# Kernel tuning notes

Measured on AMD Instinct MI355X. Metric: run time of the kernel, lower is better.

## Reference

```python
import jax, jax.numpy as jnp
import numpy as np

N = 100000   # nodes
E = 1600000  # edges
D = 128      # in_dim
H = 128      # hidden


def setup_inputs() -> dict:
    key = jax.random.key(0)
    k = jax.random.split(key, 6)
    x = jax.random.normal(k[0], (N, D), dtype=jnp.float32)
    edge_index = jax.random.randint(k[1], (2, E), 0, N, dtype=jnp.int64)
    s1 = 1.0 / np.sqrt(D)
    s2 = 1.0 / np.sqrt(H)
    W1 = jax.random.uniform(k[2], (D, H), jnp.float32, -s1, s1)
    b1 = jax.random.uniform(k[3], (H,), jnp.float32, -s1, s1)
    W2 = jax.random.uniform(k[4], (H, H), jnp.float32, -s2, s2)
    b2 = jax.random.uniform(k[5], (H,), jnp.float32, -s2, s2)
    return {"x": x, "W1": W1, "b1": b1, "W2": W2, "b2": b2,
            "edge_index": edge_index}


def reference(x, W1, b1, W2, b2, edge_index):
    n = x.shape[0]
    loop = jnp.arange(n, dtype=edge_index.dtype)
    src = jnp.concatenate([edge_index[0], loop])  # sources incl. self-loops
    dst = jnp.concatenate([edge_index[1], loop])  # targets incl. self-loops
    # symmetric GCN normalization: D^-1/2 A_hat D^-1/2
    deg = jax.ops.segment_sum(jnp.ones_like(dst, jnp.float32), dst,
                              num_segments=n)
    dinv = jnp.where(deg > 0, deg ** -0.5, 0.0)
    norm = dinv[src] * dinv[dst]  # [E+N]

    def gcn_conv(h, W, b):
        m = h @ W                                   # [N, H] transform first
        agg = jax.ops.segment_sum(norm[:, None] * m[src], dst,
                                  num_segments=n)   # gather-scale-scatter
        return agg + b

    h = jax.nn.relu(gcn_conv(x, W1, b1))  # dropout is identity in eval mode
    return gcn_conv(h, W2, b2)
```

## Files before the change

kernel.cpp:

```cpp
#include <hip/hip_runtime.h>


#define RB    9
#define RANGE 512
#define CAPB  16384
#define CHUNK 8192

typedef __attribute__((ext_vector_type(8))) short bf16x8;
typedef __attribute__((ext_vector_type(4))) float f32x4;

__device__ inline float bf_lo(unsigned w) { return __uint_as_float(w << 16); }
__device__ inline float bf_hi(unsigned w) { return __uint_as_float(w & 0xffff0000u); }
__device__ inline unsigned bf16pair(float lo, float hi) {
    unsigned a = __float_as_uint(lo), b = __float_as_uint(hi);
    a += 0x7fffu + ((a >> 16) & 1u);
    b += 0x7fffu + ((b >> 16) & 1u);
    return (a >> 16) | (b & 0xffff0000u);
}
__device__ inline unsigned short bf16rne(float f) {
    unsigned u = __float_as_uint(f);
    u += 0x7fffu + ((u >> 16) & 1u);
    return (unsigned short)(u >> 16);
}
__device__ inline float bf2f(unsigned short h) { return __uint_as_float(((unsigned)h) << 16); }

__device__ inline void pack_one(int idx, const float* __restrict__ W,
                                uint4* __restrict__ Bhi, uint4* __restrict__ Blo) {
    int lane = idx & 63, ks = (idx >> 6) & 3, nt = idx >> 8;
    int j = nt * 16 + (lane & 15);
    int k0 = ks * 32 + ((lane >> 4) & 3) * 8;
    unsigned hi[4], lo[4];
#pragma unroll
    for (int p = 0; p < 4; p++) {
        float w0 = W[(size_t)(k0 + 2 * p) * 128 + j];
        float w1 = W[(size_t)(k0 + 2 * p + 1) * 128 + j];
        unsigned short h0 = bf16rne(w0), h1 = bf16rne(w1);
        unsigned short l0 = bf16rne(w0 - bf2f(h0)), l1 = bf16rne(w1 - bf2f(h1));
        hi[p] = (unsigned)h0 | ((unsigned)h1 << 16);
        lo[p] = (unsigned)l0 | ((unsigned)l1 << 16);
    }
    Bhi[idx] = make_uint4(hi[0], hi[1], hi[2], hi[3]);
    Blo[idx] = make_uint4(lo[0], lo[1], lo[2], lo[3]);
}

__global__ __launch_bounds__(256) void setup(const unsigned* __restrict__ ei, int E,
                                             int* __restrict__ flag,
                                             unsigned* __restrict__ gcur, int NB,
                                             const float* __restrict__ W1,
                                             uint4* __restrict__ Bhi1, uint4* __restrict__ Blo1,
                                             const float* __restrict__ W2,
                                             uint4* __restrict__ Bhi2, uint4* __restrict__ Blo2) {
    const int b = blockIdx.x, t = threadIdx.x;
    if (b == 0) {
        __shared__ int nz;
        if (t == 0) nz = 0;
        __syncthreads();
        int samples = E < 2048 ? E : 2048;
        int cnt = 0;
        for (int i = t; i < samples; i += 256)
            if (ei[2 * i + 1] != 0u) cnt++;
        if (cnt) atomicAdd(&nz, cnt);
        __syncthreads();
        if (t == 0) *flag = (nz == 0) ? 1 : 0;
    } else if (b <= 2) {
        int i = (b - 1) * 256 + t;
        if (i < NB) gcur[i] = (unsigned)i * CAPB;
    } else if (b <= 10) {
        pack_one((b - 3) * 256 + t, W1, Bhi1, Blo1);
    } else {
        pack_one((b - 11) * 256 + t, W2, Bhi2, Blo2);
    }
}

__global__ __launch_bounds__(256) void bucketA(const unsigned* __restrict__ ei, int E, int n,
                                               const int* __restrict__ flag,
                                               unsigned* __restrict__ gcur,
                                               unsigned* __restrict__ recs) {
    __shared__ unsigned hist[512];
    __shared__ unsigned offs[512];
    const int t = threadIdx.x;
    const int NB = (n + RANGE - 1) >> RB;
    for (int i = t; i < NB; i += 256) hist[i] = 0u;
    __syncthreads();
    const int base = blockIdx.x * CHUNK;
    const bool i64 = (*flag != 0);
    unsigned rec[32], bk[32];
#pragma unroll
    for (int j = 0; j < 32; j++) {
        int i = base + j * 256 + t;
        unsigned bv = 0xffffffffu, rv = 0u;
        if (i < E) {
            unsigned s, d;
            if (i64) { s = ei[2 * (size_t)i]; d = ei[2 * ((size_t)E + i)]; }
            else     { s = ei[i];             d = ei[(size_t)E + i]; }
            bv = d >> RB;
            rv = (s << RB) | (d & (RANGE - 1));
            atomicAdd(&hist[bv], 1u);
        }
        rec[j] = rv; bk[j] = bv;
    }
    __syncthreads();
    for (int b = t; b < NB; b += 256) {
        unsigned h = hist[b];
        offs[b] = h ? atomicAdd(&gcur[b], h) : 0u;
    }
    __syncthreads();
#pragma unroll
    for (int j = 0; j < 32; j++) {
        unsigned b = bk[j];
        if (b != 0xffffffffu) {
            unsigned pos = atomicAdd(&offs[b], 1u);
            if (pos < (b + 1u) * CAPB) recs[pos] = rec[j];
        }
    }
}

__global__ void bscan(const unsigned* __restrict__ gcur, unsigned* __restrict__ bbase,
                      int NB, int n) {
    int lane = threadIdx.x;
    int K = (NB + 63) / 64;
    if (K > 8) K = 8;
    unsigned vals[8];
    unsigned s = 0;
#pragma unroll
    for (int k = 0; k < 8; k++) {
        vals[k] = 0u;
        int b = lane * K + k;
        if (k < K && b < NB) {
            unsigned cnt = gcur[b] - (unsigned)b * CAPB;
            if (cnt > CAPB) cnt = CAPB;
            int valid = n - (b << RB);
            if (valid > RANGE) valid = RANGE;
            if (valid < 0) valid = 0;
            vals[k] = cnt + (unsigned)valid;
        }
        s += vals[k];
    }
    unsigned inc = s;
    for (int o = 1; o < 64; o <<= 1) {
        unsigned u = (unsigned)__shfl_up((int)inc, o, 64);
        if (lane >= o) inc += u;
    }
    unsigned excl = inc - s;
#pragma unroll
    for (int k = 0; k < 8; k++) {
        int b = lane * K + k;
        if (k < K && b < NB) { bbase[b] = excl; excl += vals[k]; }
    }
}

__global__ __launch_bounds__(256) void bucket_build(const unsigned* __restrict__ gcur,
                                                    const unsigned* __restrict__ recs,
                                                    const unsigned* __restrict__ bbase,
                                                    unsigned* __restrict__ deg,
                                                    float* __restrict__ dinv,
                                                    int* __restrict__ row_off,
                                                    int* __restrict__ csr, int n) {
    __shared__ unsigned srecs[CAPB];
    __shared__ unsigned hist[RANGE];
    __shared__ unsigned lofs[RANGE];
    __shared__ int cur[RANGE];
    const int b = blockIdx.x, t = threadIdx.x;
    const int node0 = b << RB;
    unsigned base = (unsigned)b * CAPB;
    unsigned cnt = gcur[b] - base; if (cnt > CAPB) cnt = CAPB;
    for (int v = t; v < RANGE; v += 256)
        hist[v] = (node0 + v < n) ? 1u : 0u;
    __syncthreads();
    for (unsigned i = t; i < cnt; i += 256) {
        unsigned r = recs[base + i];
        srecs[i] = r;
        atomicAdd(&hist[r & (RANGE - 1)], 1u);
    }
    __syncthreads();
    if (t < 64) {
        unsigned loc[8], tot = 0;
#pragma unroll
        for (int k = 0; k < 8; k++) { unsigned h = hist[t * 8 + k]; loc[k] = tot; tot += h; }
        unsigned inc = tot;
        for (int o = 1; o < 64; o <<= 1) {
            unsigned u = (unsigned)__shfl_up((int)inc, o, 64);
            if (t >= o) inc += u;
        }
        unsigned excl = inc - tot;
#pragma unroll
        for (int k = 0; k < 8; k++) lofs[t * 8 + k] = excl + loc[k];
    }
    __syncthreads();
    unsigned bb = bbase[b];
    for (int v = t; v < RANGE; v += 256) {
        int node = node0 + v;
        if (node < n) {
            unsigned d = hist[v];
            int ro = (int)(bb + lofs[v]);
            deg[node] = d;
            dinv[node] = rsqrtf((float)d);
            row_off[node] = ro;
            csr[ro] = node;
            cur[v] = ro + 1;
        }
    }
    __syncthreads();
    for (unsigned i = t; i < cnt; i += 256) {
        unsigned r = srecs[i];
        int pos = atomicAdd(&cur[r & (RANGE - 1)], 1);
        csr[pos] = (int)(r >> RB);
    }
}

template <int SPLIT>
__global__ __launch_bounds__(256) void gemm_mfma(const void* __restrict__ Ain,
                                                 const uint4* __restrict__ Bhi,
                                                 const uint4* __restrict__ Blo,
                                                 const float* __restrict__ dinv,
                                                 unsigned short* __restrict__ Mout, int M) {
    __shared__ unsigned short Ahi[64 * 128];
    __shared__ unsigned short Alo[SPLIT ? 64 * 128 : 64];
    const int t = threadIdx.x;
    const int row0 = blockIdx.x * 64;
    char* ah8 = (char*)Ahi;
    char* al8 = (char*)Alo;

    if (SPLIT) {
        const float4* A4 = (const float4*)Ain;
#pragma unroll
        for (int it = 0; it < 4; it++) {
            int i = it * 256 + t;
            int r = i >> 4, c8 = i & 15;
            int gr = row0 + r;
            float4 v0 = make_float4(0.f, 0.f, 0.f, 0.f), v1 = v0;
            if (gr < M) { v0 = A4[(size_t)gr * 32 + c8 * 2]; v1 = A4[(size_t)gr * 32 + c8 * 2 + 1]; }
            float f[8] = {v0.x, v0.y, v0.z, v0.w, v1.x, v1.y, v1.z, v1.w};
            unsigned hp[4], lp[4];
#pragma unroll
            for (int p = 0; p < 4; p++) {
                unsigned short h0 = bf16rne(f[2 * p]), h1 = bf16rne(f[2 * p + 1]);
                unsigned short l0 = bf16rne(f[2 * p] - bf2f(h0));
                unsigned short l1 = bf16rne(f[2 * p + 1] - bf2f(h1));
                hp[p] = (unsigned)h0 | ((unsigned)h1 << 16);
                lp[p] = (unsigned)l0 | ((unsigned)l1 << 16);
            }
            int byte = (r * 256 + c8 * 16) ^ ((r & 7) << 4);
            *(uint4*)(ah8 + byte) = make_uint4(hp[0], hp[1], hp[2], hp[3]);
            *(uint4*)(al8 + byte) = make_uint4(lp[0], lp[1], lp[2], lp[3]);
        }
    } else {
        const uint4* A4 = (const uint4*)Ain;
#pragma unroll
        for (int it = 0; it < 4; it++) {
            int i = it * 256 + t;
            int r = i >> 4, c8 = i & 15;
            int gr = row0 + r;
            uint4 v = make_uint4(0u, 0u, 0u, 0u);
            if (gr < M) v = A4[(size_t)gr * 16 + c8];
            int byte = (r * 256 + c8 * 16) ^ ((r & 7) << 4);
            *(uint4*)(ah8 + byte) = v;
        }
    }
    __syncthreads();

    const int wv = t >> 6, lane = t & 63;
    const int arow = wv * 16 + (lane & 15);
    const int kh = ((lane >> 4) & 3) * 8;
    f32x4 acc[8];
#pragma unroll
    for (int nt = 0; nt < 8; nt++) acc[nt] = (f32x4){0.f, 0.f, 0.f, 0.f};
    float dv[4];
    const int orow0 = row0 + wv * 16 + ((lane >> 4) & 3) * 4;
#pragma unroll
    for (int r = 0; r < 4; r++) {
        int rr = orow0 + r;
        dv[r] = (rr < M) ? dinv[rr] : 0.f;
    }
#pragma unroll
    for (int ks = 0; ks < 4; ks++) {
        int byte = (arow * 256 + (ks * 32 + kh) * 2) ^ ((arow & 7) << 4);
        bf16x8 a_h = *(const bf16x8*)(ah8 + byte);
        bf16x8 a_l;
        if (SPLIT) a_l = *(const bf16x8*)(al8 + byte);
#pragma unroll
        for (int nt = 0; nt < 8; nt++) {
            uint4 bhv = Bhi[(nt * 4 + ks) * 64 + lane];
            uint4 blv = Blo[(nt * 4 + ks) * 64 + lane];
            bf16x8 bh = *(bf16x8*)&bhv;
            bf16x8 bl = *(bf16x8*)&blv;
            acc[nt] = __builtin_amdgcn_mfma_f32_16x16x32_bf16(a_h, bh, acc[nt], 0, 0, 0);
            if (SPLIT) acc[nt] = __builtin_amdgcn_mfma_f32_16x16x32_bf16(a_l, bh, acc[nt], 0, 0, 0);
            acc[nt] = __builtin_amdgcn_mfma_f32_16x16x32_bf16(a_h, bl, acc[nt], 0, 0, 0);
        }
    }
    __syncthreads();
#pragma unroll
    for (int nt = 0; nt < 8; nt++) {
#pragma unroll
        for (int r = 0; r < 4; r++) {
            int lr = wv * 16 + ((lane >> 4) & 3) * 4 + r;
            int byte = (lr * 256 + (nt * 16 + (lane & 15)) * 2) ^ ((lr & 7) << 4);
            *(unsigned short*)(ah8 + byte) = bf16rne(acc[nt][r] * dv[r]);
        }
    }
    __syncthreads();
#pragma unroll
    for (int it = 0; it < 4; it++) {
        int i = it * 256 + t;
        int r = i >> 4, c8 = i & 15;
        int gr = row0 + r;
        if (gr < M) {
            int byte = (r * 256 + c8 * 16) ^ ((r & 7) << 4);
            *(uint4*)(Mout + (size_t)gr * 128 + c8 * 8) = *(uint4*)(ah8 + byte);
        }
    }
}

__global__ __launch_bounds__(256) void agg_kernel(const unsigned* __restrict__ m,
                                                  const int* __restrict__ csr,
                                                  const int* __restrict__ row_off,
                                                  const unsigned* __restrict__ deg,
                                                  const float* __restrict__ dinv,
                                                  const float* __restrict__ bias,
                                                  void* __restrict__ outp, int n, int mode) {
    int wid = threadIdx.x >> 6, lane = threadIdx.x & 63;
    int v = blockIdx.x * 4 + wid;
    if (v >= n) return;
    int start = row_off[v];
    int cnt = (int)deg[v];
    float ax = 0.f, ay = 0.f;
    int e = 0;
    while (e < cnt) {
        int nload = cnt - e;
        if (nload > 64) nload = 64;
        int sv = 0;
        if (lane < nload) sv = csr[start + e + lane];
        int j = 0;
        for (; j + 16 <= nload; j += 16) {
            unsigned w[16];
#pragma unroll
            for (int q = 0; q < 16; q++) {
                int s = __shfl(sv, j + q);
                w[q] = m[(size_t)s * 64 + lane];
            }
#pragma unroll
            for (int q = 0; q < 16; q++) { ax += bf_lo(w[q]); ay += bf_hi(w[q]); }
        }
        if (j + 8 <= nload) {
            unsigned w[8];
#pragma unroll
            for (int q = 0; q < 8; q++) {
                int s = __shfl(sv, j + q);
                w[q] = m[(size_t)s * 64 + lane];
            }
#pragma unroll
            for (int q = 0; q < 8; q++) { ax += bf_lo(w[q]); ay += bf_hi(w[q]); }
            j += 8;
        }
        for (; j < nload; j++) {
            int s = __shfl(sv, j);
            unsigned w = m[(size_t)s * 64 + lane];
            ax += bf_lo(w); ay += bf_hi(w);
        }
        e += nload;
    }
    float dv = dinv[v];
    float2 b = ((const float2*)bias)[lane];
    float ox = fmaf(dv, ax, b.x), oy = fmaf(dv, ay, b.y);
    if (mode) {
        ox = fmaxf(ox, 0.f); oy = fmaxf(oy, 0.f);
        ((unsigned*)outp)[(size_t)v * 64 + lane] = bf16pair(ox, oy);
    } else {
        ((float2*)outp)[(size_t)v * 64 + lane] = make_float2(ox, oy);
    }
}

extern "C" void kernel_launch(void* const* d_in, const int* in_sizes, int n_in,
                              void* d_out, int out_size, void* d_ws, size_t ws_size,
                              hipStream_t stream) {
    const float*    x  = (const float*)d_in[0];
    const float*    W1 = (const float*)d_in[1];
    const float*    b1 = (const float*)d_in[2];
    const float*    W2 = (const float*)d_in[3];
    const float*    b2 = (const float*)d_in[4];
    const unsigned* ei = (const unsigned*)d_in[5];
    int n = in_sizes[0] / 128;
    int E = in_sizes[5] / 2;
    float* out = (float*)d_out;
    int NB = (n + RANGE - 1) >> RB;

    char* w = (char*)d_ws;
    size_t off = 0;
    auto alloc = [&](size_t bytes) -> void* {
        void* p = w + off;
        off = (off + bytes + 255) & ~(size_t)255;
        return p;
    };
    int*            flag     = (int*)alloc(4);
    unsigned*       deg      = (unsigned*)alloc((size_t)n * 4);
    float*          dinv     = (float*)alloc((size_t)n * 4);
    int*            row_off  = (int*)alloc((size_t)(n + 1) * 4);
    unsigned*       bbase    = (unsigned*)alloc(512 * 4);
    unsigned*       gcur     = (unsigned*)alloc(512 * 4);
    uint4*          Bhi1     = (uint4*)alloc(2048 * 16);
    uint4*          Blo1     = (uint4*)alloc(2048 * 16);
    uint4*          Bhi2     = (uint4*)alloc(2048 * 16);
    uint4*          Blo2     = (uint4*)alloc(2048 * 16);
    unsigned*       recs     = (unsigned*)alloc((size_t)NB * CAPB * 4);
    int*            csr      = (int*)alloc((size_t)(E + n + 64) * 4);
    unsigned short* m_bf     = (unsigned short*)alloc((size_t)n * 128 * 2);
    unsigned*       h_bf     = (unsigned*)alloc((size_t)n * 64 * 4);
    (void)ws_size; (void)n_in; (void)out_size;

    int nchunk = (E + CHUNK - 1) / CHUNK;

    hipLaunchKernelGGL(setup, dim3(19), dim3(256), 0, stream,
                       ei, E, flag, gcur, NB, W1, Bhi1, Blo1, W2, Bhi2, Blo2);
    hipLaunchKernelGGL(bucketA, dim3(nchunk), dim3(256), 0, stream, ei, E, n, flag, gcur, recs);
    hipLaunchKernelGGL(bscan, dim3(1), dim3(64), 0, stream, gcur, bbase, NB, n);
    hipLaunchKernelGGL(bucket_build, dim3(NB), dim3(256), 0, stream,
                       gcur, recs, bbase, deg, dinv, row_off, csr, n);

    int gblocks = (n + 63) / 64;
    hipLaunchKernelGGL((gemm_mfma<1>), dim3(gblocks), dim3(256), 0, stream,
                       (const void*)x, Bhi1, Blo1, dinv, m_bf, n);
    hipLaunchKernelGGL(agg_kernel, dim3((n + 3) / 4), dim3(256), 0, stream,
                       (const unsigned*)m_bf, csr, row_off, deg, dinv, b1, (void*)h_bf, n, 1);
    hipLaunchKernelGGL((gemm_mfma<0>), dim3(gblocks), dim3(256), 0, stream,
                       (const void*)h_bf, Bhi2, Blo2, dinv, m_bf, n);
    hipLaunchKernelGGL(agg_kernel, dim3((n + 3) / 4), dim3(256), 0, stream,
                       (const unsigned*)m_bf, csr, row_off, deg, dinv, b2, (void*)out, n, 0);
}
```

Baseline: 236.5 us.

## Repartition GEMM waves over column tiles with register-cached B fragments

Each wave of the MFMA GEMM now owns two of the eight 16-column output tiles and loops over the four 16-row chunks, instead of owning 16 rows and all eight column tiles. Its B fragments are loaded from global memory once into registers before the first barrier, so the global load latency overlaps the A staging and B is not re-fetched inside the MFMA loop. Output goes through a small padded shared staging buffer one 16-row chunk at a time, which costs an extra barrier pair per chunk and re-reads of A from shared memory by every wave.

```diff
diff --git a/kernel.cpp b/kernel.cpp
--- a/kernel.cpp
+++ b/kernel.cpp
@@ -216,6 +216,7 @@
                                                  unsigned short* __restrict__ Mout, int M) {
     __shared__ unsigned short Ahi[64 * 128];
     __shared__ unsigned short Alo[SPLIT ? 64 * 128 : 64];
+    __shared__ unsigned short Cst[16 * 136];
     const int t = threadIdx.x;
     const int row0 = blockIdx.x * 64;
     char* ah8 = (char*)Ahi;
@@ -257,58 +258,63 @@
             *(uint4*)(ah8 + byte) = v;
         }
     }
-    __syncthreads();
 
     const int wv = t >> 6, lane = t & 63;
-    const int arow = wv * 16 + (lane & 15);
     const int kh = ((lane >> 4) & 3) * 8;
-    f32x4 acc[8];
-#pragma unroll
-    for (int nt = 0; nt < 8; nt++) acc[nt] = (f32x4){0.f, 0.f, 0.f, 0.f};
-    float dv[4];
-    const int orow0 = row0 + wv * 16 + ((lane >> 4) & 3) * 4;
-#pragma unroll
-    for (int r = 0; r < 4; r++) {
-        int rr = orow0 + r;
-        dv[r] = (rr < M) ? dinv[rr] : 0.f;
-    }
-#pragma unroll
-    for (int ks = 0; ks < 4; ks++) {
-        int byte = (arow * 256 + (ks * 32 + kh) * 2) ^ ((arow & 7) << 4);
-        bf16x8 a_h = *(const bf16x8*)(ah8 + byte);
-        bf16x8 a_l;
-        if (SPLIT) a_l = *(const bf16x8*)(al8 + byte);
-#pragma unroll
-        for (int nt = 0; nt < 8; nt++) {
-            uint4 bhv = Bhi[(nt * 4 + ks) * 64 + lane];
-            uint4 blv = Blo[(nt * 4 + ks) * 64 + lane];
-            bf16x8 bh = *(bf16x8*)&bhv;
-            bf16x8 bl = *(bf16x8*)&blv;
-            acc[nt] = __builtin_amdgcn_mfma_f32_16x16x32_bf16(a_h, bh, acc[nt], 0, 0, 0);
-            if (SPLIT) acc[nt] = __builtin_amdgcn_mfma_f32_16x16x32_bf16(a_l, bh, acc[nt], 0, 0, 0);
-            acc[nt] = __builtin_amdgcn_mfma_f32_16x16x32_bf16(a_h, bl, acc[nt], 0, 0, 0);
-        }
-    }
-    __syncthreads();
-#pragma unroll
-    for (int nt = 0; nt < 8; nt++) {
+    const int lr0 = ((lane >> 4) & 3) * 4;
+    uint4 bhv[2][4], blv[2][4];
+#pragma unroll
+    for (int p = 0; p < 2; p++)
+#pragma unroll
+        for (int ks = 0; ks < 4; ks++) {
+            int nt = wv * 2 + p;
+            bhv[p][ks] = Bhi[(nt * 4 + ks) * 64 + lane];
+            blv[p][ks] = Blo[(nt * 4 + ks) * 64 + lane];
+        }
+    __syncthreads();
+
+#pragma unroll
+    for (int c = 0; c < 4; c++) {
+        f32x4 acc[2];
+        acc[0] = (f32x4){0.f, 0.f, 0.f, 0.f};
+        acc[1] = (f32x4){0.f, 0.f, 0.f, 0.f};
+        const int arow = c * 16 + (lane & 15);
+#pragma unroll
+        for (int ks = 0; ks < 4; ks++) {
+            int byte = (arow * 256 + (ks * 32 + kh) * 2) ^ ((arow & 7) << 4);
+            bf16x8 a_h = *(const bf16x8*)(ah8 + byte);
+            bf16x8 a_l;
+            if (SPLIT) a_l = *(const bf16x8*)(al8 + byte);
+#pragma unroll
+            for (int p = 0; p < 2; p++) {
+                bf16x8 bh = *(bf16x8*)&bhv[p][ks];
+                bf16x8 bl = *(bf16x8*)&blv[p][ks];
+                acc[p] = __builtin_amdgcn_mfma_f32_16x16x32_bf16(a_h, bh, acc[p], 0, 0, 0);
+                if (SPLIT) acc[p] = __builtin_amdgcn_mfma_f32_16x16x32_bf16(a_l, bh, acc[p], 0, 0, 0);
+                acc[p] = __builtin_amdgcn_mfma_f32_16x16x32_bf16(a_h, bl, acc[p], 0, 0, 0);
+            }
+        }
+        float dvr[4];
 #pragma unroll
         for (int r = 0; r < 4; r++) {
-            int lr = wv * 16 + ((lane >> 4) & 3) * 4 + r;
-            int byte = (lr * 256 + (nt * 16 + (lane & 15)) * 2) ^ ((lr & 7) << 4);
-            *(unsigned short*)(ah8 + byte) = bf16rne(acc[nt][r] * dv[r]);
-        }
-    }
-    __syncthreads();
-#pragma unroll
-    for (int it = 0; it < 4; it++) {
-        int i = it * 256 + t;
-        int r = i >> 4, c8 = i & 15;
-        int gr = row0 + r;
-        if (gr < M) {
-            int byte = (r * 256 + c8 * 16) ^ ((r & 7) << 4);
-            *(uint4*)(Mout + (size_t)gr * 128 + c8 * 8) = *(uint4*)(ah8 + byte);
-        }
+            int grow = row0 + c * 16 + lr0 + r;
+            dvr[r] = (grow < M) ? dinv[grow] : 0.f;
+        }
+#pragma unroll
+        for (int p = 0; p < 2; p++) {
+            int nt = wv * 2 + p;
+#pragma unroll
+            for (int r = 0; r < 4; r++)
+                Cst[(lr0 + r) * 136 + nt * 16 + (lane & 15)] = bf16rne(acc[p][r] * dvr[r]);
+        }
+        __syncthreads();
+        {
+            int r = t >> 4, c8 = t & 15;
+            int gr = row0 + c * 16 + r;
+            if (gr < M)
+                *(uint4*)(Mout + (size_t)gr * 128 + c8 * 8) = *(uint4*)&Cst[r * 136 + c8 * 8];
+        }
+        __syncthreads();
     }
 }
 
```

Result: faster. 222.9 us, median of 2 (-5.8%).
